# Kernel tuning notes

Measured on AMD Instinct MI355X. Metric: run time of the kernel, lower is better.

The kernel has to match this reference:

```python
import jax, jax.numpy as jnp
import numpy as np

H = 512   # hidden_size
V = 5000  # output_size (vocab)
B = 128   # batch
S = 64    # encoder source length
T = 52    # max_trajectory_length


def setup_inputs() -> dict:
    key = jax.random.key(0)
    ks = jax.random.split(key, 16)
    sc = 0.05
    rn = lambda k, shape: jax.random.normal(k, shape, dtype=jnp.float32) * sc
    return dict(
        encoder_outputs=jax.random.normal(ks[0], (B, S, H), dtype=jnp.float32),
        h0=jax.random.normal(ks[1], (1, B, H), dtype=jnp.float32),
        c0=jax.random.normal(ks[2], (1, B, H), dtype=jnp.float32),
        target_tensor=jax.random.randint(ks[3], (B, T), 0, V),
        emb=rn(ks[4], (V, H)),
        Wa=rn(ks[5], (H, H)), ba=jnp.zeros((H,), jnp.float32),
        Ua=rn(ks[6], (H, H)), bu=jnp.zeros((H,), jnp.float32),
        Va=rn(ks[7], (H,)), bv=jnp.zeros((), jnp.float32),
        W_ih=rn(ks[8], (4 * H, 2 * H)), W_hh=rn(ks[9], (4 * H, H)),
        b_ih=jnp.zeros((4 * H,), jnp.float32), b_hh=jnp.zeros((4 * H,), jnp.float32),
        Wout=rn(ks[10], (V, H)), bout=jnp.zeros((V,), jnp.float32),
    )


def reference(encoder_outputs, h0, c0, target_tensor, emb,
              Wa, ba, Ua, bu, Va, bv,
              W_ih, W_hh, b_ih, b_hh, Wout, bout):
    # Dropout is identity in eval mode.
    b = target_tensor.shape[0]
    # Ua(keys) is constant across decode steps -> precompute once. [B,S,H]
    keys_proj = jnp.einsum('bsh,kh->bsk', encoder_outputs, Ua) + bu
    # Teacher forcing: input at step i is target[:, i-1], step 0 is token 0.
    tokens = jnp.concatenate(
        [jnp.zeros((b, 1), target_tensor.dtype), target_tensor[:, :-1]], axis=1)  # [B,T]

    def step(carry, tok):
        h, c = carry                                # [B,H] each
        x = emb[tok]                                # embedding lookup [B,H]
        q = h @ Wa.T + ba                           # Wa(query) [B,H]
        scores = jnp.tanh(q[:, None, :] + keys_proj) @ Va + bv  # [B,S]
        w = jax.nn.softmax(scores, axis=-1)         # attn weights [B,S]
        ctx = jnp.einsum('bs,bsh->bh', w, encoder_outputs)       # context [B,H]
        xi = jnp.concatenate([x, ctx], axis=-1)     # [B,2H]
        gates = xi @ W_ih.T + b_ih + h @ W_hh.T + b_hh           # [B,4H]
        i_g, f_g, g_g, o_g = jnp.split(gates, 4, axis=-1)        # torch gate order i,f,g,o
        c = jax.nn.sigmoid(f_g) * c + jax.nn.sigmoid(i_g) * jnp.tanh(g_g)
        h = jax.nn.sigmoid(o_g) * jnp.tanh(c)
        logits = h @ Wout.T + bout                  # [B,V]
        return (h, c), (logits, w)

    (h, c), (logits, attn) = jax.lax.scan(step, (h0[0], c0[0]), tokens.T)
    logits = jnp.transpose(logits, (1, 0, 2))       # [B,T,V]
    log_probs = jax.nn.log_softmax(logits, axis=-1)
    attn = jnp.transpose(attn, (1, 0, 2))           # [B,T,S]
    return log_probs, (h[None], c[None]), attn
```

## Files before the change

kernel.cpp:

```cpp
#include <hip/hip_runtime.h>
#include <math.h>

#define H 512
#define V 5000
#define BB 128
#define SS 64
#define TT 52
#define NB 160

typedef __attribute__((ext_vector_type(8))) short bf16x8;
typedef __attribute__((ext_vector_type(4))) float f32x4;
typedef __attribute__((ext_vector_type(2))) float f32x2;

__device__ __forceinline__ unsigned short f2b(float f) {
    unsigned u = __float_as_uint(f);
    return (unsigned short)((u + 0x7fffu + ((u >> 16) & 1u)) >> 16);
}
__device__ __forceinline__ float b2f(unsigned short u) {
    return __uint_as_float((unsigned)u << 16);
}
__device__ __forceinline__ float ftanh(float x) {
    return 1.f - 2.f / (1.f + __expf(2.f * x));
}
__device__ __forceinline__ float fsig(float x) {
    return 1.f / (1.f + __expf(-x));
}
__device__ __forceinline__ unsigned char f2fp8(float f) {
    return (unsigned char)__builtin_amdgcn_cvt_pk_fp8_f32(f, f, 0, 0);
}

#define CLD16_BODY \
        "global_load_dwordx4 %0, %16, off sc0 sc1\n\t"              \
        "global_load_dwordx4 %1, %16, off offset:64 sc0 sc1\n\t"    \
        "global_load_dwordx4 %2, %16, off offset:128 sc0 sc1\n\t"   \
        "global_load_dwordx4 %3, %16, off offset:192 sc0 sc1\n\t"   \
        "global_load_dwordx4 %4, %16, off offset:256 sc0 sc1\n\t"   \
        "global_load_dwordx4 %5, %16, off offset:320 sc0 sc1\n\t"   \
        "global_load_dwordx4 %6, %16, off offset:384 sc0 sc1\n\t"   \
        "global_load_dwordx4 %7, %16, off offset:448 sc0 sc1\n\t"   \
        "global_load_dwordx4 %8, %16, off offset:512 sc0 sc1\n\t"   \
        "global_load_dwordx4 %9, %16, off offset:576 sc0 sc1\n\t"   \
        "global_load_dwordx4 %10, %16, off offset:640 sc0 sc1\n\t"  \
        "global_load_dwordx4 %11, %16, off offset:704 sc0 sc1\n\t"  \
        "global_load_dwordx4 %12, %16, off offset:768 sc0 sc1\n\t"  \
        "global_load_dwordx4 %13, %16, off offset:832 sc0 sc1\n\t"  \
        "global_load_dwordx4 %14, %16, off offset:896 sc0 sc1\n\t"  \
        "global_load_dwordx4 %15, %16, off offset:960 sc0 sc1"
#define CLD16_OUTS(r) \
          "=v"(r[0]), "=v"(r[1]), "=v"(r[2]), "=v"(r[3]),   \
          "=v"(r[4]), "=v"(r[5]), "=v"(r[6]), "=v"(r[7]),   \
          "=v"(r[8]), "=v"(r[9]), "=v"(r[10]), "=v"(r[11]), \
          "=v"(r[12]), "=v"(r[13]), "=v"(r[14]), "=v"(r[15])

__device__ __forceinline__ void cld_row16_nw(const unsigned short* p, bf16x8* r)
{
    asm volatile(CLD16_BODY : CLD16_OUTS(r) : "v"(p) : "memory");
}
__device__ __forceinline__ void cld_row16(const unsigned short* p, bf16x8* r)
{
    asm volatile(CLD16_BODY "\n\ts_waitcnt vmcnt(0)"
                 : CLD16_OUTS(r) : "v"(p) : "memory");
}
__device__ __forceinline__ void cld_f_2(const float* p0, const float* p1,
                                        float& a, float& b)
{
    asm volatile(
        "global_load_dword %0, %2, off sc0 sc1\n\t"
        "global_load_dword %1, %3, off sc0 sc1\n\t"
        "s_waitcnt vmcnt(0)"
        : "=v"(a), "=v"(b) : "v"(p0), "v"(p1) : "memory");
}
__device__ __forceinline__ void cld_f4p(const float* p, f32x4& a, f32x4& b)
{
    asm volatile(
        "global_load_dwordx4 %0, %2, off sc0 sc1\n\t"
        "global_load_dwordx4 %1, %2, off offset:16 sc0 sc1\n\t"
        "s_waitcnt vmcnt(0)"
        : "=v"(a), "=v"(b) : "v"(p) : "memory");
}
__device__ __forceinline__ void cst_f(float* p, float v)
{
    asm volatile("global_store_dword %0, %1, off sc0 sc1"
                 :: "v"(p), "v"(v) : "memory");
}
__device__ __forceinline__ void cst_u32(unsigned* p, unsigned v)
{
    asm volatile("global_store_dword %0, %1, off sc0 sc1"
                 :: "v"(p), "v"(v) : "memory");
}
__device__ __forceinline__ void cst_h(unsigned short* p, unsigned short v)
{
    unsigned vv = v;
    asm volatile("global_store_short %0, %1, off sc0 sc1"
                 :: "v"(p), "v"(vv) : "memory");
}

__global__ __launch_bounds__(256)
void prep_w(const float* __restrict__ Wa, const float* __restrict__ Whh,
            const float* __restrict__ Wih,
            const float* __restrict__ ba, const float* __restrict__ bih,
            const float* __restrict__ bhh,
            const float* __restrict__ Ua, const float* __restrict__ Wout,
            const float* __restrict__ enc,
            unsigned short* __restrict__ Wbig, unsigned short* __restrict__ Wc,
            unsigned short* __restrict__ Uab, unsigned short* __restrict__ Woutb,
            unsigned short* __restrict__ encb, float* __restrict__ bbig)
{
    const int stride = gridDim.x * blockDim.x;
    const int t0 = blockIdx.x * blockDim.x + threadIdx.x;
    for (int idx = t0; idx < 2560 * 1024; idx += stride) {
        const int j = idx >> 10, k = idx & 1023;
        float v;
        if (j < H) v = (k < H) ? Wa[j * H + k] : 0.f;
        else { const int n = j - H; v = (k < H) ? Whh[n * H + k] : Wih[n * 2 * H + (k - H)]; }
        Wbig[idx] = f2b(v);
    }
    for (int idx = t0; idx < 2048 * 512; idx += stride) {
        const int n = idx >> 9, k = idx & 511;
        Wc[idx] = f2b(Wih[n * 2 * H + H + k]);
    }
    for (int idx = t0; idx < 512 * 512; idx += stride)   Uab[idx]   = f2b(Ua[idx]);
    for (int idx = t0; idx < V * 512; idx += stride)     Woutb[idx] = f2b(Wout[idx]);
    for (int idx = t0; idx < BB * SS * H; idx += stride) encb[idx]  = f2b(enc[idx]);
    for (int j = t0; j < 2560; j += stride)
        bbig[j] = (j < H) ? ba[j] : bih[j - H] + bhh[j - H];
}

__global__ __launch_bounds__(256)
void gather_x(const float* __restrict__ emb, const int* __restrict__ tgt,
              unsigned short* __restrict__ xall)
{
    const int stride = gridDim.x * blockDim.x;
    for (int idx = blockIdx.x * blockDim.x + threadIdx.x; idx < TT * BB * H; idx += stride) {
        const int k = idx & 511;
        const int row = idx >> 9;
        const int t = row >> 7, b = row & 127;
        const int tok = (t == 0) ? 0 : tgt[b * TT + t - 1];
        xall[idx] = f2b(emb[(size_t)tok * H + k]);
    }
}

template<int OUT_MODE, int PERMUTE>
__global__ __launch_bounds__(256, 2)
void gemm_mfma(const unsigned short* __restrict__ A,
               const unsigned short* __restrict__ B,
               const float* __restrict__ bias,
               float* __restrict__ Cf, unsigned short* __restrict__ Cb,
               unsigned char* __restrict__ C8,
               int M, int N)
{
    __shared__ unsigned short As[128][72];
    __shared__ unsigned short Bs[128][72];
    const int tid = threadIdx.x;
    const int m0 = blockIdx.y * 128, n0 = blockIdx.x * 128;
    const int lane = tid & 63, wv = tid >> 6;
    const int qm = (wv >> 1) * 64, qn = (wv & 1) * 64;
    const int fr = lane & 15, fg = lane >> 4;
    f32x4 acc[4][4];
#pragma unroll
    for (int i = 0; i < 4; ++i)
#pragma unroll
        for (int j = 0; j < 4; ++j) acc[i][j] = (f32x4){0.f, 0.f, 0.f, 0.f};

    const int srow = tid >> 3, sc = (tid & 7) * 8;
    for (int k0 = 0; k0 < H; k0 += 64) {
#pragma unroll
        for (int u = 0; u < 4; ++u) {
            const int row = srow + u * 32;
            *(uint4*)&As[row][sc] = *(const uint4*)&A[(size_t)(m0 + row) * H + k0 + sc];
            int nr = n0 + row; if (nr > N - 1) nr = N - 1;
            *(uint4*)&Bs[row][sc] = *(const uint4*)&B[(size_t)nr * H + k0 + sc];
        }
        __syncthreads();
#pragma unroll
        for (int ks = 0; ks < 2; ++ks) {
            const int kk = ks * 32 + fg * 8;
            bf16x8 av[4], bv[4];
#pragma unroll
            for (int i = 0; i < 4; ++i) {
                av[i] = *(const bf16x8*)&As[qm + i * 16 + fr][kk];
                bv[i] = *(const bf16x8*)&Bs[qn + i * 16 + fr][kk];
            }
#pragma unroll
            for (int i = 0; i < 4; ++i)
#pragma unroll
                for (int j = 0; j < 4; ++j)
                    acc[i][j] = __builtin_amdgcn_mfma_f32_16x16x32_bf16(av[i], bv[j], acc[i][j], 0, 0, 0);
        }
        __syncthreads();
    }
#pragma unroll
    for (int i = 0; i < 4; ++i) {
        const int r0 = m0 + qm + i * 16 + fg * 4;
#pragma unroll
        for (int j = 0; j < 4; ++j) {
            const int col = n0 + qn + j * 16 + fr;
            if (col < N) {
                const float bi = bias ? bias[col] : 0.f;
#pragma unroll
                for (int v = 0; v < 4; ++v) {
                    const int r = r0 + v;
                    const float val = acc[i][j][v] + bi;
                    if (OUT_MODE == 1) {
                        Cb[(size_t)r * N + col] = f2b(val);
                    } else if (OUT_MODE == 2) {
                        C8[(size_t)r * N + col] = f2fp8(val);
                    } else {
                        const size_t orow = PERMUTE ? ((size_t)(r & (BB - 1)) * TT + (r >> 7))
                                                    : (size_t)r;
                        Cf[orow * (size_t)N + col] = val;
                    }
                }
            }
        }
    }
}

__device__ __forceinline__ void poll_ge(unsigned* a, unsigned step)
{
    if (__hip_atomic_load(a, __ATOMIC_RELAXED, __HIP_MEMORY_SCOPE_AGENT) >= step)
        return;
    do {
        __builtin_amdgcn_s_sleep(2);
    } while (__hip_atomic_load(a, __ATOMIC_RELAXED, __HIP_MEMORY_SCOPE_AGENT) < step);
}

struct PParams {
    const float* h0;
    const float* c0;
    const unsigned short* keysb;
    const unsigned char* encW8;
    const float* Va;
    const float* bv;
    const float* bbig;
    const unsigned short* Wbig;
    const unsigned short* xall;
    unsigned short* hbf;
    float* Y;
    unsigned short* hallb;
    float* attn;
    float* out_h;
    float* out_c;
    unsigned* pflag;
    unsigned* qaflag;
    unsigned* gateflag;
    unsigned* hflag;
};

__global__ __launch_bounds__(256, 1)
void persist(PParams p)
{
    __shared__ unsigned short WA[16][1032];
    __shared__ float qa_s[H];
    __shared__ float va_s[H];
    __shared__ float part[SS][4];
    __shared__ float wbuf[SS];
    __shared__ float gbuf[4 * H];
    __shared__ float cs[H];

    const int tid  = threadIdx.x;
    const int beta = blockIdx.x;
    const int rep  = beta & 7;
    const int j0   = (beta < 128) ? (512 + beta * 16) : ((beta - 128) * 16);

    for (int i = beta * 256 + tid; i < BB * H; i += NB * 256)
        cst_h(&p.hbf[i], f2b(p.h0[i]));
    for (int idx = tid; idx < 16 * 128; idx += 256) {
        const int r = idx >> 7, ch = idx & 127;
        *(uint4*)&WA[r][ch * 8] = *(const uint4*)&p.Wbig[(size_t)(j0 + r) * 1024 + ch * 8];
    }
    if (beta < 128) {
        for (int j = tid; j < H; j += 256) cs[j] = p.c0[beta * H + j];
        for (int i = tid; i < H; i += 256) va_s[i] = p.Va[i];
    }
    __syncthreads();
    if (tid == 0)
        __hip_atomic_store(&p.pflag[beta * 32], 1u, __ATOMIC_RELAXED,
                           __HIP_MEMORY_SCOPE_AGENT);
    for (int i = tid; i < NB; i += 256) poll_ge(&p.pflag[i * 32], 1u);
    __syncthreads();

    for (int t = 0; t < TT; ++t) {
        const unsigned st = (unsigned)(t + 1);
        {
            const int wv = tid >> 6, lane = tid & 63;
            const int r = lane & 15, g = lane >> 4;
            const int b0 = wv * 32, b1 = b0 + 16;
            const int ko = g * 8;
            if (t > 0 && lane < 32)
                poll_ge(&p.hflag[(rep * 128 + b0 + lane) * 32], (unsigned)t);
            bf16x8 hr0[16], hr1[16];
            cld_row16_nw(p.hbf + (size_t)(b0 + r) * H + ko, hr0);
            cld_row16  (p.hbf + (size_t)(b1 + r) * H + ko, hr1);
            __builtin_amdgcn_sched_barrier(0);
            f32x4 acc0 = {0.f, 0.f, 0.f, 0.f};
            f32x4 acc1 = {0.f, 0.f, 0.f, 0.f};
#pragma unroll
            for (int ks = 0; ks < 16; ++ks) {
                bf16x8 bf = *(const bf16x8*)&WA[r][ks * 32 + ko];
                acc0 = __builtin_amdgcn_mfma_f32_16x16x32_bf16(hr0[ks], bf, acc0, 0, 0, 0);
                acc1 = __builtin_amdgcn_mfma_f32_16x16x32_bf16(hr1[ks], bf, acc1, 0, 0, 0);
            }
            const unsigned short* x0p = p.xall + ((size_t)t * BB + b0 + r) * H + ko;
            const unsigned short* x1p = p.xall + ((size_t)t * BB + b1 + r) * H + ko;
#pragma unroll
            for (int ks = 0; ks < 16; ++ks) {
                bf16x8 bf = *(const bf16x8*)&WA[r][512 + ks * 32 + ko];
                acc0 = __builtin_amdgcn_mfma_f32_16x16x32_bf16(*(const bf16x8*)&x0p[ks * 32], bf, acc0, 0, 0, 0);
                acc1 = __builtin_amdgcn_mfma_f32_16x16x32_bf16(*(const bf16x8*)&x1p[ks * 32], bf, acc1, 0, 0, 0);
            }
            const float bb = p.bbig[j0 + r];
#pragma unroll
            for (int i = 0; i < 4; ++i) {
                cst_f(p.Y + (size_t)(b0 + g * 4 + i) * 2560 + j0 + r, acc0[i] + bb);
                cst_f(p.Y + (size_t)(b1 + g * 4 + i) * 2560 + j0 + r, acc1[i] + bb);
            }
        }
        __syncthreads();
        if (tid < 8) {
            if (beta < 128)
                __hip_atomic_store(&p.gateflag[(tid * 128 + beta) * 32], st,
                                   __ATOMIC_RELAXED, __HIP_MEMORY_SCOPE_AGENT);
            else
                __hip_atomic_store(&p.qaflag[(tid * 32 + beta - 128) * 32], st,
                                   __ATOMIC_RELAXED, __HIP_MEMORY_SCOPE_AGENT);
        }

        if (beta < 128) {
            const int b = beta;
            const float* yrow = p.Y + (size_t)b * 2560;
            if (tid < 32) poll_ge(&p.qaflag[(rep * 32 + tid) * 32], st);
            __syncthreads();
            cld_f_2(yrow + tid, yrow + 256 + tid, qa_s[tid], qa_s[tid + 256]);
            __syncthreads();
            const int s = tid >> 2, q = tid & 3;
            const unsigned short* kp = p.keysb + ((size_t)b * SS + s) * H + q * 128;
            const float* qp = qa_s + q * 128;
            const float* vp = va_s + q * 128;
            float a2 = 0.f, a2b = 0.f;
#pragma unroll
            for (int i8 = 0; i8 < 16; ++i8) {
                bf16x8 kv = *(const bf16x8*)&kp[i8 * 8];
#pragma unroll
                for (int u = 0; u < 8; u += 2) {
                    const int i = i8 * 8 + u;
                    a2  += ftanh(qp[i]     + b2f((unsigned short)kv[u]))     * vp[i];
                    a2b += ftanh(qp[i + 1] + b2f((unsigned short)kv[u + 1])) * vp[i + 1];
                }
            }
            part[s][q] = a2 + a2b;
            __syncthreads();
            if (tid < 64) {
                float sc = part[tid][0] + part[tid][1] + part[tid][2] + part[tid][3] + p.bv[0];
                float m = sc;
                for (int o = 32; o; o >>= 1) m = fmaxf(m, __shfl_xor(m, o));
                const float e = __expf(sc - m);
                float ss = e;
                for (int o = 32; o; o >>= 1) ss += __shfl_xor(ss, o);
                const float w = e / ss;
                wbuf[tid] = w;
                p.attn[((size_t)b * TT + t) * SS + tid] = w;
            }
            if (tid < 128) poll_ge(&p.gateflag[(rep * 128 + tid) * 32], st);
            __syncthreads();
            {
                float gc[8] = {0.f, 0.f, 0.f, 0.f, 0.f, 0.f, 0.f, 0.f};
                const unsigned char* ew = p.encW8 + (size_t)b * SS * 2048 + tid * 8;
#pragma unroll 8
                for (int s2 = 0; s2 < SS; ++s2) {
                    const float w2 = wbuf[s2];
                    const uint2 u = *(const uint2*)(ew + (size_t)s2 * 2048);
                    const f32x2 e01 = __builtin_amdgcn_cvt_pk_f32_fp8(u.x, 0);
                    const f32x2 e23 = __builtin_amdgcn_cvt_pk_f32_fp8(u.x, 1);
                    const f32x2 e45 = __builtin_amdgcn_cvt_pk_f32_fp8(u.y, 0);
                    const f32x2 e67 = __builtin_amdgcn_cvt_pk_f32_fp8(u.y, 1);
                    gc[0] += w2 * e01[0]; gc[1] += w2 * e01[1];
                    gc[2] += w2 * e23[0]; gc[3] += w2 * e23[1];
                    gc[4] += w2 * e45[0]; gc[5] += w2 * e45[1];
                    gc[6] += w2 * e67[0]; gc[7] += w2 * e67[1];
                }
                f32x4 y0, y1;
                cld_f4p(yrow + 512 + tid * 8, y0, y1);
#pragma unroll
                for (int i = 0; i < 4; ++i) {
                    gbuf[tid * 8 + i]     = gc[i] + y0[i];
                    gbuf[tid * 8 + 4 + i] = gc[4 + i] + y1[i];
                }
            }
            __syncthreads();
            {
                const int last = (t == TT - 1);
                unsigned hpack = 0;
                float hn2[2], cn2[2];
#pragma unroll
                for (int u = 0; u < 2; ++u) {
                    const int j = tid * 2 + u;
                    const float ig = gbuf[j];
                    const float fg = gbuf[512 + j];
                    const float gg = gbuf[1024 + j];
                    const float og = gbuf[1536 + j];
                    const float co = cs[j];
                    const float cn = fsig(fg) * co + fsig(ig) * ftanh(gg);
                    const float hn = fsig(og) * ftanh(cn);
                    cs[j] = cn;
                    hn2[u] = hn; cn2[u] = cn;
                    hpack |= ((unsigned)f2b(hn)) << (16 * u);
                }
                cst_u32((unsigned*)&p.hbf[b * H + tid * 2], hpack);
                *(unsigned*)&p.hallb[((size_t)t * BB + b) * H + tid * 2] = hpack;
                if (last) {
#pragma unroll
                    for (int u = 0; u < 2; ++u) {
                        p.out_h[b * H + tid * 2 + u] = hn2[u];
                        p.out_c[b * H + tid * 2 + u] = cn2[u];
                    }
                }
            }
            __syncthreads();
            if (tid < 8)
                __hip_atomic_store(&p.hflag[(tid * 128 + beta) * 32], st,
                                   __ATOMIC_RELAXED, __HIP_MEMORY_SCOPE_AGENT);
        }
    }
}

__global__ __launch_bounds__(256)
void logsoftmax_rows(float* __restrict__ P)
{
    __shared__ float red[256];
    float* p = P + (size_t)blockIdx.x * V;
    const int tid = threadIdx.x;
    float m = -1e30f;
    for (int i = tid; i < V; i += 256) m = fmaxf(m, p[i]);
    red[tid] = m; __syncthreads();
    for (int sft = 128; sft; sft >>= 1) {
        if (tid < sft) red[tid] = fmaxf(red[tid], red[tid + sft]);
        __syncthreads();
    }
    m = red[0]; __syncthreads();
    float ssum = 0.f;
    for (int i = tid; i < V; i += 256) ssum += __expf(p[i] - m);
    red[tid] = ssum; __syncthreads();
    for (int sft = 128; sft; sft >>= 1) {
        if (tid < sft) red[tid] += red[tid + sft];
        __syncthreads();
    }
    const float lse = m + __logf(red[0]);
    for (int i = tid; i < V; i += 256) p[i] -= lse;
}

extern "C" void kernel_launch(void* const* d_in, const int* in_sizes, int n_in,
                              void* d_out, int out_size, void* d_ws, size_t ws_size,
                              hipStream_t stream)
{
    (void)in_sizes; (void)n_in; (void)out_size; (void)ws_size;
    const float* enc  = (const float*)d_in[0];
    const float* h0   = (const float*)d_in[1];
    const float* c0   = (const float*)d_in[2];
    const int*   tgt  = (const int*)  d_in[3];
    const float* emb  = (const float*)d_in[4];
    const float* Wa   = (const float*)d_in[5];
    const float* ba   = (const float*)d_in[6];
    const float* Ua   = (const float*)d_in[7];
    const float* bu   = (const float*)d_in[8];
    const float* Va   = (const float*)d_in[9];
    const float* bv   = (const float*)d_in[10];
    const float* Wih  = (const float*)d_in[11];
    const float* Whh  = (const float*)d_in[12];
    const float* bih  = (const float*)d_in[13];
    const float* bhh  = (const float*)d_in[14];
    const float* Wout = (const float*)d_in[15];
    const float* bout = (const float*)d_in[16];

    float* ws = (float*)d_ws;
    float* Y    = ws;
    float* bbig = Y + 327680;
    unsigned* flags = (unsigned*)(bbig + 2560);
    unsigned* pflag    = flags;
    unsigned* qaflag   = flags + 5120;
    unsigned* gateflag = flags + 13312;
    unsigned* hflag    = flags + 46080;
    unsigned short* Wbig  = (unsigned short*)(flags + 78848);
    unsigned short* Wc    = Wbig + 2621440;
    unsigned short* Uab   = Wc + 1048576;
    unsigned short* Woutb = Uab + 262144;
    unsigned short* encb  = Woutb + 2560000;
    unsigned short* keysb = encb + 4194304;
    unsigned short* xall  = keysb + 4194304;
    unsigned short* hallb = xall + 3407872;
    unsigned short* hbf   = hallb + 3407872;
    unsigned char*  encW8 = (unsigned char*)(hbf + 65536);

    float* out    = (float*)d_out;
    float* out_h  = out + (size_t)BB * TT * V;
    float* out_c  = out_h + BB * H;
    float* out_at = out_c + BB * H;

    hipMemsetAsync(flags, 0, 78848 * sizeof(unsigned), stream);

    prep_w<<<dim3(2048), dim3(256), 0, stream>>>(
        Wa, Whh, Wih, ba, bih, bhh, Ua, Wout, enc, Wbig, Wc, Uab, Woutb, encb, bbig);
    gather_x<<<dim3(512), dim3(256), 0, stream>>>(emb, tgt, xall);

    gemm_mfma<1, 0><<<dim3(4, 64), dim3(256), 0, stream>>>(
        encb, Uab, bu, nullptr, keysb, nullptr, BB * SS, H);
    gemm_mfma<2, 0><<<dim3(16, 64), dim3(256), 0, stream>>>(
        encb, Wc, nullptr, nullptr, nullptr, encW8, BB * SS, 2048);

    PParams pp;
    pp.h0 = h0; pp.c0 = c0; pp.keysb = keysb; pp.encW8 = encW8;
    pp.Va = Va; pp.bv = bv; pp.bbig = bbig;
    pp.Wbig = Wbig; pp.xall = xall;
    pp.hbf = hbf; pp.Y = Y; pp.hallb = hallb;
    pp.attn = out_at; pp.out_h = out_h; pp.out_c = out_c;
    pp.pflag = pflag; pp.qaflag = qaflag; pp.gateflag = gateflag; pp.hflag = hflag;
    persist<<<dim3(NB), dim3(256), 0, stream>>>(pp);

    gemm_mfma<0, 1><<<dim3(40, 52), dim3(256), 0, stream>>>(
        hallb, Woutb, bout, out, nullptr, nullptr, TT * BB, V);
    logsoftmax_rows<<<dim3(BB * TT), dim3(256), 0, stream>>>(out);
}
```

Measured before the change: 1.468 ms.

## Fuse output projection into persistent kernel on idle query blocks, transpose gate buffer

The separate output-projection GEMM is removed. Its work now runs inside the persistent LSTM kernel: the 32 query-attention blocks (beta>=128) compute the logits for step t-1 while the batch blocks handle step t, and they compute the final step after the loop. The gate buffer Y is stored transposed (column-major by batch) so that each block writes one vectorised store. The replicated flag arrays are collapsed to a single flag per block, and the poll sleep is shortened. The change is meant to hide the logits GEMM behind the serial recurrence. In exchange it loads A and B operands directly from global memory without LDS tiling, and the extra work on the query blocks may lengthen the critical path, since every step waits on qaflag.

After: 2.396 ms. +63.2%, slower.

```diff
diff --git a/kernel.cpp b/kernel.cpp
--- a/kernel.cpp
+++ b/kernel.cpp
@@ -70,17 +70,25 @@
         "s_waitcnt vmcnt(0)"
         : "=v"(a), "=v"(b) : "v"(p0), "v"(p1) : "memory");
 }
-__device__ __forceinline__ void cld_f4p(const float* p, f32x4& a, f32x4& b)
+__device__ __forceinline__ void cld_f8s(const float* p, float* r)
 {
     asm volatile(
-        "global_load_dwordx4 %0, %2, off sc0 sc1\n\t"
-        "global_load_dwordx4 %1, %2, off offset:16 sc0 sc1\n\t"
+        "global_load_dword %0, %8, off sc0 sc1\n\t"
+        "global_load_dword %1, %8, off offset:512 sc0 sc1\n\t"
+        "global_load_dword %2, %8, off offset:1024 sc0 sc1\n\t"
+        "global_load_dword %3, %8, off offset:1536 sc0 sc1\n\t"
+        "global_load_dword %4, %8, off offset:2048 sc0 sc1\n\t"
+        "global_load_dword %5, %8, off offset:2560 sc0 sc1\n\t"
+        "global_load_dword %6, %8, off offset:3072 sc0 sc1\n\t"
+        "global_load_dword %7, %8, off offset:3584 sc0 sc1\n\t"
         "s_waitcnt vmcnt(0)"
-        : "=v"(a), "=v"(b) : "v"(p) : "memory");
-}
-__device__ __forceinline__ void cst_f(float* p, float v)
-{
-    asm volatile("global_store_dword %0, %1, off sc0 sc1"
+        : "=v"(r[0]), "=v"(r[1]), "=v"(r[2]), "=v"(r[3]),
+          "=v"(r[4]), "=v"(r[5]), "=v"(r[6]), "=v"(r[7])
+        : "v"(p) : "memory");
+}
+__device__ __forceinline__ void cst_f4(float* p, f32x4 v)
+{
+    asm volatile("global_store_dwordx4 %0, %1, off sc0 sc1"
                  :: "v"(p), "v"(v) : "memory");
 }
 __device__ __forceinline__ void cst_u32(unsigned* p, unsigned v)
@@ -140,12 +148,12 @@
     }
 }
 
-template<int OUT_MODE, int PERMUTE>
+template<int OUT_MODE>
 __global__ __launch_bounds__(256, 2)
 void gemm_mfma(const unsigned short* __restrict__ A,
                const unsigned short* __restrict__ B,
                const float* __restrict__ bias,
-               float* __restrict__ Cf, unsigned short* __restrict__ Cb,
+               unsigned short* __restrict__ Cb,
                unsigned char* __restrict__ C8,
                int M, int N)
 {
@@ -201,15 +209,8 @@
                 for (int v = 0; v < 4; ++v) {
                     const int r = r0 + v;
                     const float val = acc[i][j][v] + bi;
-                    if (OUT_MODE == 1) {
-                        Cb[(size_t)r * N + col] = f2b(val);
-                    } else if (OUT_MODE == 2) {
-                        C8[(size_t)r * N + col] = f2fp8(val);
-                    } else {
-                        const size_t orow = PERMUTE ? ((size_t)(r & (BB - 1)) * TT + (r >> 7))
-                                                    : (size_t)r;
-                        Cf[orow * (size_t)N + col] = val;
-                    }
+                    if (OUT_MODE == 1) Cb[(size_t)r * N + col] = f2b(val);
+                    else               C8[(size_t)r * N + col] = f2fp8(val);
                 }
             }
         }
@@ -221,7 +222,7 @@
     if (__hip_atomic_load(a, __ATOMIC_RELAXED, __HIP_MEMORY_SCOPE_AGENT) >= step)
         return;
     do {
-        __builtin_amdgcn_s_sleep(2);
+        __builtin_amdgcn_s_sleep(1);
     } while (__hip_atomic_load(a, __ATOMIC_RELAXED, __HIP_MEMORY_SCOPE_AGENT) < step);
 }
 
@@ -233,12 +234,15 @@
     const float* Va;
     const float* bv;
     const float* bbig;
+    const float* bout;
     const unsigned short* Wbig;
+    const unsigned short* Woutb;
     const unsigned short* xall;
     unsigned short* hbf;
-    float* Y;
+    float* Yt;
     unsigned short* hallb;
     float* attn;
+    float* out;
     float* out_h;
     float* out_c;
     unsigned* pflag;
@@ -260,8 +264,9 @@
 
     const int tid  = threadIdx.x;
     const int beta = blockIdx.x;
-    const int rep  = beta & 7;
     const int j0   = (beta < 128) ? (512 + beta * 16) : ((beta - 128) * 16);
+    const int wv   = tid >> 6, lane = tid & 63;
+    const int fr   = lane & 15, fg = lane >> 4;
 
     for (int i = beta * 256 + tid; i < BB * H; i += NB * 256)
         cst_h(&p.hbf[i], f2b(p.h0[i]));
@@ -283,12 +288,11 @@
     for (int t = 0; t < TT; ++t) {
         const unsigned st = (unsigned)(t + 1);
         {
-            const int wv = tid >> 6, lane = tid & 63;
-            const int r = lane & 15, g = lane >> 4;
+            const int r = fr, g = fg;
             const int b0 = wv * 32, b1 = b0 + 16;
             const int ko = g * 8;
             if (t > 0 && lane < 32)
-                poll_ge(&p.hflag[(rep * 128 + b0 + lane) * 32], (unsigned)t);
+                poll_ge(&p.hflag[(b0 + lane) * 32], (unsigned)t);
             bf16x8 hr0[16], hr1[16];
             cld_row16_nw(p.hbf + (size_t)(b0 + r) * H + ko, hr0);
             cld_row16  (p.hbf + (size_t)(b1 + r) * H + ko, hr1);
@@ -310,28 +314,79 @@
                 acc1 = __builtin_amdgcn_mfma_f32_16x16x32_bf16(*(const bf16x8*)&x1p[ks * 32], bf, acc1, 0, 0, 0);
             }
             const float bb = p.bbig[j0 + r];
-#pragma unroll
-            for (int i = 0; i < 4; ++i) {
-                cst_f(p.Y + (size_t)(b0 + g * 4 + i) * 2560 + j0 + r, acc0[i] + bb);
-                cst_f(p.Y + (size_t)(b1 + g * 4 + i) * 2560 + j0 + r, acc1[i] + bb);
-            }
+            f32x4 o0, o1;
+#pragma unroll
+            for (int i = 0; i < 4; ++i) { o0[i] = acc0[i] + bb; o1[i] = acc1[i] + bb; }
+            cst_f4(p.Yt + (size_t)(j0 + r) * BB + b0 + g * 4, o0);
+            cst_f4(p.Yt + (size_t)(j0 + r) * BB + b1 + g * 4, o1);
         }
         __syncthreads();
-        if (tid < 8) {
+        if (tid == 0) {
             if (beta < 128)
-                __hip_atomic_store(&p.gateflag[(tid * 128 + beta) * 32], st,
-                                   __ATOMIC_RELAXED, __HIP_MEMORY_SCOPE_AGENT);
+                __hip_atomic_store(&p.gateflag[beta * 32], st, __ATOMIC_RELAXED,
+                                   __HIP_MEMORY_SCOPE_AGENT);
             else
-                __hip_atomic_store(&p.qaflag[(tid * 32 + beta - 128) * 32], st,
-                                   __ATOMIC_RELAXED, __HIP_MEMORY_SCOPE_AGENT);
+                __hip_atomic_store(&p.qaflag[(beta - 128) * 32], st, __ATOMIC_RELAXED,
+                                   __HIP_MEMORY_SCOPE_AGENT);
         }
 
-        if (beta < 128) {
+        if (beta >= 128) {
+            if (t > 0) {
+                const int tl = t - 1;
+                const int lb = beta - 128;
+#pragma unroll
+                for (int pass = 0; pass < 2; ++pass) {
+                    const int nb = lb * 160 + pass * 80;
+                    const int mg0 = 32 * wv, mg1 = mg0 + 16;
+                    const unsigned short* A0 = p.hallb + ((size_t)tl * BB + mg0 + fr) * H;
+                    const unsigned short* A1 = p.hallb + ((size_t)tl * BB + mg1 + fr) * H;
+                    const unsigned short* Bp[5];
+#pragma unroll
+                    for (int cg = 0; cg < 5; ++cg) {
+                        int nr = nb + cg * 16 + fr; if (nr > V - 1) nr = V - 1;
+                        Bp[cg] = p.Woutb + (size_t)nr * H;
+                    }
+                    f32x4 acc[2][5];
+#pragma unroll
+                    for (int i = 0; i < 2; ++i)
+#pragma unroll
+                        for (int cg = 0; cg < 5; ++cg) acc[i][cg] = (f32x4){0.f, 0.f, 0.f, 0.f};
+#pragma unroll
+                    for (int ks = 0; ks < 16; ++ks) {
+                        const int kk = ks * 32 + fg * 8;
+                        bf16x8 a0 = *(const bf16x8*)&A0[kk];
+                        bf16x8 a1 = *(const bf16x8*)&A1[kk];
+#pragma unroll
+                        for (int cg = 0; cg < 5; ++cg) {
+                            bf16x8 bb = *(const bf16x8*)&Bp[cg][kk];
+                            acc[0][cg] = __builtin_amdgcn_mfma_f32_16x16x32_bf16(a0, bb, acc[0][cg], 0, 0, 0);
+                            acc[1][cg] = __builtin_amdgcn_mfma_f32_16x16x32_bf16(a1, bb, acc[1][cg], 0, 0, 0);
+                        }
+                    }
+#pragma unroll
+                    for (int i = 0; i < 2; ++i) {
+                        const int mg = (i == 0) ? mg0 : mg1;
+#pragma unroll
+                        for (int cg = 0; cg < 5; ++cg) {
+                            const int col = nb + cg * 16 + fr;
+                            if (col < V) {
+                                const float bo = p.bout[col];
+#pragma unroll
+                                for (int v = 0; v < 4; ++v) {
+                                    const int bt = mg + fg * 4 + v;
+                                    p.out[((size_t)bt * TT + tl) * V + col] = acc[i][cg][v] + bo;
+                                }
+                            }
+                        }
+                    }
+                }
+            }
+        } else {
             const int b = beta;
-            const float* yrow = p.Y + (size_t)b * 2560;
-            if (tid < 32) poll_ge(&p.qaflag[(rep * 32 + tid) * 32], st);
+            if (tid < 32) poll_ge(&p.qaflag[tid * 32], st);
             __syncthreads();
-            cld_f_2(yrow + tid, yrow + 256 + tid, qa_s[tid], qa_s[tid + 256]);
+            cld_f_2(p.Yt + (size_t)tid * BB + b, p.Yt + (size_t)(tid + 256) * BB + b,
+                    qa_s[tid], qa_s[tid + 256]);
             __syncthreads();
             const int s = tid >> 2, q = tid & 3;
             const unsigned short* kp = p.keysb + ((size_t)b * SS + s) * H + q * 128;
@@ -361,7 +416,7 @@
                 wbuf[tid] = w;
                 p.attn[((size_t)b * TT + t) * SS + tid] = w;
             }
-            if (tid < 128) poll_ge(&p.gateflag[(rep * 128 + tid) * 32], st);
+            if (tid < 128) poll_ge(&p.gateflag[tid * 32], st);
             __syncthreads();
             {
                 float gc[8] = {0.f, 0.f, 0.f, 0.f, 0.f, 0.f, 0.f, 0.f};
@@ -379,13 +434,11 @@
                     gc[4] += w2 * e45[0]; gc[5] += w2 * e45[1];
                     gc[6] += w2 * e67[0]; gc[7] += w2 * e67[1];
                 }
-                f32x4 y0, y1;
-                cld_f4p(yrow + 512 + tid * 8, y0, y1);
-#pragma unroll
-                for (int i = 0; i < 4; ++i) {
-                    gbuf[tid * 8 + i]     = gc[i] + y0[i];
-                    gbuf[tid * 8 + 4 + i] = gc[4 + i] + y1[i];
-                }
+                float yg[8];
+                cld_f8s(p.Yt + (size_t)(512 + tid * 8) * BB + b, yg);
+#pragma unroll
+                for (int i = 0; i < 8; ++i)
+                    gbuf[tid * 8 + i] = gc[i] + yg[i];
             }
             __syncthreads();
             {
@@ -396,18 +449,18 @@
                 for (int u = 0; u < 2; ++u) {
                     const int j = tid * 2 + u;
                     const float ig = gbuf[j];
-                    const float fg = gbuf[512 + j];
+                    const float fgt = gbuf[512 + j];
                     const float gg = gbuf[1024 + j];
                     const float og = gbuf[1536 + j];
                     const float co = cs[j];
-                    const float cn = fsig(fg) * co + fsig(ig) * ftanh(gg);
+                    const float cn = fsig(fgt) * co + fsig(ig) * ftanh(gg);
                     const float hn = fsig(og) * ftanh(cn);
                     cs[j] = cn;
                     hn2[u] = hn; cn2[u] = cn;
                     hpack |= ((unsigned)f2b(hn)) << (16 * u);
                 }
                 cst_u32((unsigned*)&p.hbf[b * H + tid * 2], hpack);
-                *(unsigned*)&p.hallb[((size_t)t * BB + b) * H + tid * 2] = hpack;
+                cst_u32((unsigned*)&p.hallb[((size_t)t * BB + b) * H + tid * 2], hpack);
                 if (last) {
 #pragma unroll
                     for (int u = 0; u < 2; ++u) {
@@ -417,9 +470,62 @@
                 }
             }
             __syncthreads();
-            if (tid < 8)
-                __hip_atomic_store(&p.hflag[(tid * 128 + beta) * 32], st,
-                                   __ATOMIC_RELAXED, __HIP_MEMORY_SCOPE_AGENT);
+            if (tid == 0)
+                __hip_atomic_store(&p.hflag[beta * 32], st, __ATOMIC_RELAXED,
+                                   __HIP_MEMORY_SCOPE_AGENT);
+        }
+    }
+
+    if (beta >= 128) {
+        for (int i = tid; i < 128; i += 256) poll_ge(&p.hflag[i * 32], (unsigned)TT);
+        __syncthreads();
+        const int tl = TT - 1;
+        const int lb = beta - 128;
+#pragma unroll
+        for (int pass = 0; pass < 2; ++pass) {
+            const int nb = lb * 160 + pass * 80;
+            const int mg0 = 32 * wv, mg1 = mg0 + 16;
+            const unsigned short* A0 = p.hallb + ((size_t)tl * BB + mg0 + fr) * H;
+            const unsigned short* A1 = p.hallb + ((size_t)tl * BB + mg1 + fr) * H;
+            const unsigned short* Bp[5];
+#pragma unroll
+            for (int cg = 0; cg < 5; ++cg) {
+                int nr = nb + cg * 16 + fr; if (nr > V - 1) nr = V - 1;
+                Bp[cg] = p.Woutb + (size_t)nr * H;
+            }
+            f32x4 acc[2][5];
+#pragma unroll
+            for (int i = 0; i < 2; ++i)
+#pragma unroll
+                for (int cg = 0; cg < 5; ++cg) acc[i][cg] = (f32x4){0.f, 0.f, 0.f, 0.f};
+#pragma unroll
+            for (int ks = 0; ks < 16; ++ks) {
+                const int kk = ks * 32 + fg * 8;
+                bf16x8 a0 = *(const bf16x8*)&A0[kk];
+                bf16x8 a1 = *(const bf16x8*)&A1[kk];
+#pragma unroll
+                for (int cg = 0; cg < 5; ++cg) {
+                    bf16x8 bb = *(const bf16x8*)&Bp[cg][kk];
+                    acc[0][cg] = __builtin_amdgcn_mfma_f32_16x16x32_bf16(a0, bb, acc[0][cg], 0, 0, 0);
+                    acc[1][cg] = __builtin_amdgcn_mfma_f32_16x16x32_bf16(a1, bb, acc[1][cg], 0, 0, 0);
+                }
+            }
+#pragma unroll
+            for (int i = 0; i < 2; ++i) {
+                const int mg = (i == 0) ? mg0 : mg1;
+#pragma unroll
+                for (int cg = 0; cg < 5; ++cg) {
+                    const int col = nb + cg * 16 + fr;
+                    if (col < V) {
+                        const float bo = p.bout[col];
+#pragma unroll
+                        for (int v = 0; v < 4; ++v) {
+                            const int bt = mg + fg * 4 + v;
+                            p.out[((size_t)bt * TT + tl) * V + col] = acc[i][cg][v] + bo;
+                        }
+                    }
+                }
+            }
         }
     }
 }
@@ -473,14 +579,14 @@
     const float* bout = (const float*)d_in[16];
 
     float* ws = (float*)d_ws;
-    float* Y    = ws;
-    float* bbig = Y + 327680;
+    float* Yt   = ws;
+    float* bbig = Yt + 327680;
     unsigned* flags = (unsigned*)(bbig + 2560);
     unsigned* pflag    = flags;
     unsigned* qaflag   = flags + 5120;
-    unsigned* gateflag = flags + 13312;
-    unsigned* hflag    = flags + 46080;
-    unsigned short* Wbig  = (unsigned short*)(flags + 78848);
+    unsigned* gateflag = flags + 6144;
+    unsigned* hflag    = flags + 10240;
+    unsigned short* Wbig  = (unsigned short*)(flags + 14336);
     unsigned short* Wc    = Wbig + 2621440;
     unsigned short* Uab   = Wc + 1048576;
     unsigned short* Woutb = Uab + 262144;
@@ -496,27 +602,25 @@
     float* out_c  = out_h + BB * H;
     float* out_at = out_c + BB * H;
 
-    hipMemsetAsync(flags, 0, 78848 * sizeof(unsigned), stream);
+    hipMemsetAsync(flags, 0, 14336 * sizeof(unsigned), stream);
 
     prep_w<<<dim3(2048), dim3(256), 0, stream>>>(
         Wa, Whh, Wih, ba, bih, bhh, Ua, Wout, enc, Wbig, Wc, Uab, Woutb, encb, bbig);
     gather_x<<<dim3(512), dim3(256), 0, stream>>>(emb, tgt, xall);
 
-    gemm_mfma<1, 0><<<dim3(4, 64), dim3(256), 0, stream>>>(
-        encb, Uab, bu, nullptr, keysb, nullptr, BB * SS, H);
-    gemm_mfma<2, 0><<<dim3(16, 64), dim3(256), 0, stream>>>(
-        encb, Wc, nullptr, nullptr, nullptr, encW8, BB * SS, 2048);
+    gemm_mfma<1><<<dim3(4, 64), dim3(256), 0, stream>>>(
+        encb, Uab, bu, keysb, nullptr, BB * SS, H);
+    gemm_mfma<2><<<dim3(16, 64), dim3(256), 0, stream>>>(
+        encb, Wc, nullptr, nullptr, encW8, BB * SS, 2048);
 
     PParams pp;
     pp.h0 = h0; pp.c0 = c0; pp.keysb = keysb; pp.encW8 = encW8;
-    pp.Va = Va; pp.bv = bv; pp.bbig = bbig;
-    pp.Wbig = Wbig; pp.xall = xall;
-    pp.hbf = hbf; pp.Y = Y; pp.hallb = hallb;
-    pp.attn = out_at; pp.out_h = out_h; pp.out_c = out_c;
+    pp.Va = Va; pp.bv = bv; pp.bbig = bbig; pp.bout = bout;
+    pp.Wbig = Wbig; pp.Woutb = Woutb; pp.xall = xall;
+    pp.hbf = hbf; pp.Yt = Yt; pp.hallb = hallb;
+    pp.attn = out_at; pp.out = out; pp.out_h = out_h; pp.out_c = out_c;
     pp.pflag = pflag; pp.qaflag = qaflag; pp.gateflag = gateflag; pp.hflag = hflag;
     persist<<<dim3(NB), dim3(256), 0, stream>>>(pp);
 
-    gemm_mfma<0, 1><<<dim3(40, 52), dim3(256), 0, stream>>>(
-        hallb, Woutb, bout, out, nullptr, nullptr, TT * BB, V);
     logsoftmax_rows<<<dim3(BB * TT), dim3(256), 0, stream>>>(out);
 }
```
